# Performance work log

Measured on AMD Instinct MI355X. Metric: run time of the kernel, lower is better.

The kernel has to match this reference:

```python
import jax, jax.numpy as jnp
import numpy as np


def setup_inputs() -> dict:
    key = jax.random.key(0)
    k1, k2 = jax.random.split(key)
    B, T, D = 32, 512, 384
    x = jax.random.normal(k1, (B, T, D), dtype=jnp.float32)
    duration = jax.random.randint(k2, (B, T), 0, 8, dtype=jnp.int32)
    max_length = 4096  # T * max_duration, worst-case expanded mel length
    return {"x": x, "duration": duration, "max_length": max_length}


def reference(x, duration, max_length):
    # x: [B, T, D] float; duration: [B, T] int; returns padded expanded
    # sequence [B, M, D] and mel positions [B, M] (1-based, 0 for padding).
    B, T, D = x.shape
    cum = jnp.cumsum(duration, axis=1)          # [B, T] cumulative frame offsets
    total = cum[:, -1]                          # [B] total mel frames per batch
    frames = jnp.arange(max_length)             # [M]
    # For output frame j, source token = first i with cum[i] > j
    tok = jax.vmap(lambda c: jnp.searchsorted(c, frames, side='right'))(cum)  # [B, M]
    tok = jnp.clip(tok, 0, T - 1)
    valid = frames[None, :] < total[:, None]    # [B, M]
    out = jnp.take_along_axis(x, tok[:, :, None], axis=1)   # [B, M, D]
    out = out * valid[:, :, None].astype(x.dtype)            # zero-pad tail
    mel_pos = jnp.where(valid, frames[None, :] + 1, 0)       # [B, M]
    return out, mel_pos
```

## Files before the change

### kernel.cpp

```cpp
#include <hip/hip_runtime.h>


constexpr int B  = 32;
constexpr int T  = 512;
constexpr int D  = 384;
constexpr int ML = 4096;
constexpr int D4 = D / 4;
constexpr int FPB = 128;
constexpr int BLOCKS_PER_BATCH = ML / FPB;
constexpr int NT = 256;

__global__ __launch_bounds__(NT) void lr_kernel(
        const float4* __restrict__ x,
        const int*    __restrict__ dur,
        float*        __restrict__ outf,
        float*        __restrict__ mel)
{
    __shared__ int s_cum[T];
    __shared__ int s_tok[FPB];
    __shared__ int s_part[NT];

    const int b      = blockIdx.x / BLOCKS_PER_BATCH;
    const int fchunk = blockIdx.x % BLOCKS_PER_BATCH;
    const int f0     = fchunk * FPB;
    const int tid    = threadIdx.x;

    const int d0 = dur[b * T + 2 * tid];
    const int d1 = dur[b * T + 2 * tid + 1];
    const int pair = d0 + d1;
    s_part[tid] = pair;
    __syncthreads();
    int val = pair;
    #pragma unroll
    for (int off = 1; off < NT; off <<= 1) {
        int t = (tid >= off) ? s_part[tid - off] : 0;
        __syncthreads();
        val += t;
        s_part[tid] = val;
        __syncthreads();
    }
    const int excl = val - pair;
    s_cum[2 * tid]     = excl + d0;
    s_cum[2 * tid + 1] = excl + pair;
    __syncthreads();
    const int total = s_cum[T - 1];

    if (tid < FPB) {
        const int f = f0 + tid;
        int lo = 0, hi = T;
        while (lo < hi) {
            const int mid = (lo + hi) >> 1;
            if (s_cum[mid] <= f) lo = mid + 1; else hi = mid;
        }
        const int tok = (lo < T - 1) ? lo : (T - 1);
        s_tok[tid] = (f < total) ? tok : -1;
        mel[b * ML + f] = (f < total) ? (float)(f + 1) : 0.0f;
    }
    __syncthreads();

    float4* __restrict__ out4 = (float4*)outf;
    const float4 zero4 = make_float4(0.f, 0.f, 0.f, 0.f);
    const size_t out_base = ((size_t)b * ML + f0) * D4;
    const size_t x_base   = (size_t)b * T * D4;
    #pragma unroll 4
    for (int i = tid; i < FPB * D4; i += NT) {
        const int lf  = i / D4;
        const int c   = i - lf * D4;
        const int tok = s_tok[lf];
        float4 v = zero4;
        if (tok >= 0) v = x[x_base + (size_t)tok * D4 + c];
        out4[out_base + (size_t)lf * D4 + c] = v;
    }
}

extern "C" void kernel_launch(void* const* d_in, const int* in_sizes, int n_in,
                              void* d_out, int out_size, void* d_ws, size_t ws_size,
                              hipStream_t stream) {
    const float4* x   = (const float4*)d_in[0];
    const int*    dur = (const int*)d_in[1];
    float* outf = (float*)d_out;
    float* mel  = outf + (size_t)B * ML * D;

    dim3 grid(B * BLOCKS_PER_BATCH);
    dim3 block(NT);
    lr_kernel<<<grid, block, 0, stream>>>(x, dur, outf, mel);
}
```

Baseline: 232.7 us.

## Halve frames per block, add zero-tail fast path, nontemporal stores

```diff
diff --git a/kernel.cpp b/kernel.cpp
--- a/kernel.cpp
+++ b/kernel.cpp
@@ -1,20 +1,23 @@
 #include <hip/hip_runtime.h>
 
+
+typedef float v4f __attribute__((ext_vector_type(4)));
 
 constexpr int B  = 32;
 constexpr int T  = 512;
 constexpr int D  = 384;
 constexpr int ML = 4096;
 constexpr int D4 = D / 4;
-constexpr int FPB = 128;
+constexpr int FPB = 64;
 constexpr int BLOCKS_PER_BATCH = ML / FPB;
 constexpr int NT = 256;
+constexpr int ITERS = FPB * D4 / NT;
 
 __global__ __launch_bounds__(NT) void lr_kernel(
-        const float4* __restrict__ x,
-        const int*    __restrict__ dur,
-        float*        __restrict__ outf,
-        float*        __restrict__ mel)
+        const v4f* __restrict__ x,
+        const int* __restrict__ dur,
+        v4f*       __restrict__ out4,
+        float*     __restrict__ mel)
 {
     __shared__ int s_cum[T];
     __shared__ int s_tok[FPB];
@@ -45,6 +48,19 @@
     __syncthreads();
     const int total = s_cum[T - 1];
 
+    const v4f zero4 = (v4f){0.f, 0.f, 0.f, 0.f};
+    v4f* op = out4 + ((size_t)b * ML + f0) * D4 + tid;
+
+    if (f0 >= total) {
+        if (tid < FPB) mel[b * ML + f0 + tid] = 0.0f;
+        #pragma unroll
+        for (int k = 0; k < ITERS; ++k) {
+            __builtin_nontemporal_store(zero4, op);
+            op += NT;
+        }
+        return;
+    }
+
     if (tid < FPB) {
         const int f = f0 + tid;
         int lo = 0, hi = T;
@@ -58,30 +74,31 @@
     }
     __syncthreads();
 
-    float4* __restrict__ out4 = (float4*)outf;
-    const float4 zero4 = make_float4(0.f, 0.f, 0.f, 0.f);
-    const size_t out_base = ((size_t)b * ML + f0) * D4;
-    const size_t x_base   = (size_t)b * T * D4;
-    #pragma unroll 4
-    for (int i = tid; i < FPB * D4; i += NT) {
-        const int lf  = i / D4;
-        const int c   = i - lf * D4;
+    const v4f* xb = x + (size_t)b * T * D4;
+    int i  = tid;
+    int lf = i / D4;
+    int c  = i - lf * D4;
+    #pragma unroll
+    for (int k = 0; k < ITERS; ++k) {
         const int tok = s_tok[lf];
-        float4 v = zero4;
-        if (tok >= 0) v = x[x_base + (size_t)tok * D4 + c];
-        out4[out_base + (size_t)lf * D4 + c] = v;
+        v4f v = zero4;
+        if (tok >= 0) v = xb[tok * D4 + c];
+        __builtin_nontemporal_store(v, op);
+        op += NT;
+        lf += 2; c += NT - 2 * D4;
+        if (c >= D4) { c -= D4; ++lf; }
     }
 }
 
 extern "C" void kernel_launch(void* const* d_in, const int* in_sizes, int n_in,
                               void* d_out, int out_size, void* d_ws, size_t ws_size,
                               hipStream_t stream) {
-    const float4* x   = (const float4*)d_in[0];
-    const int*    dur = (const int*)d_in[1];
+    const v4f* x    = (const v4f*)d_in[0];
+    const int* dur  = (const int*)d_in[1];
     float* outf = (float*)d_out;
     float* mel  = outf + (size_t)B * ML * D;
 
     dim3 grid(B * BLOCKS_PER_BATCH);
     dim3 block(NT);
-    lr_kernel<<<grid, block, 0, stream>>>(x, dur, outf, mel);
+    lr_kernel<<<grid, block, 0, stream>>>(x, dur, (v4f*)outf, mel);
 }
```

Measured after the change: 241.8 us. 3.9% more time.
